# Optimization experiments

Measured on AMD Instinct MI355X. Metric: run time of the kernel, lower is better.

Reference implementation:

```python
import jax, jax.numpy as jnp
import numpy as np

B, S, P = 2, 1024, 1024          # batch, new tokens, cached (past) tokens
H, NQ, NKV, D = 4096, 32, 8, 128  # hidden, q heads, kv heads, head dim
G = NQ // NKV                     # GQA group size
SCALE = 1.0 / np.sqrt(D)


def _make_rope(positions, dim, base=10000.0):
    inv = 1.0 / (base ** (np.arange(0, dim, 2, dtype=np.float32) / dim))
    freqs = positions[:, None].astype(np.float32) * inv[None, :]
    emb = np.concatenate([freqs, freqs], axis=-1)  # [S, D]
    return jnp.asarray(np.cos(emb)), jnp.asarray(np.sin(emb))


def setup_inputs() -> dict:
    key = jax.random.key(0)
    ks = jax.random.split(key, 5)
    hidden_states = jax.random.normal(ks[0], (B, S, H), jnp.float32)
    w_qkv = jax.random.normal(ks[1], (H, (NQ + 2 * NKV) * D), jnp.float32) * 0.02
    w_o = jax.random.normal(ks[2], (NQ * D, H), jnp.float32) * 0.02
    cos, sin = _make_rope(np.arange(P, P + S), D)  # new tokens at positions P..P+S-1
    k_cache = jax.random.normal(ks[3], (B, P, NKV, D), jnp.float32)
    v_cache = jax.random.normal(ks[4], (B, P, NKV, D), jnp.float32)
    return dict(hidden_states=hidden_states, w_qkv=w_qkv, w_o=w_o,
                cos=cos, sin=sin, k_cache=k_cache, v_cache=v_cache)


def _rotate_half(x):
    x1, x2 = jnp.split(x, 2, axis=-1)
    return jnp.concatenate([-x2, x1], axis=-1)


def _apply_rope(x, cos, sin):
    # x: [B,S,N,D]; cos/sin: [S,D]
    return x * cos[None, :, None, :] + _rotate_half(x) * sin[None, :, None, :]


def reference(hidden_states, w_qkv, w_o, cos, sin, k_cache, v_cache):
    # fused QKV projection
    qkv = hidden_states @ w_qkv                       # [B,S,(NQ+2*NKV)*D]
    q, k, v = jnp.split(qkv, [NQ * D, (NQ + NKV) * D], axis=-1)
    q = q.reshape(B, S, NQ, D)
    k = k.reshape(B, S, NKV, D)
    v = v.reshape(B, S, NKV, D)
    # inline RoPE on q and k
    q = _apply_rope(q, cos, sin)
    k = _apply_rope(k, cos, sin)
    # append new k/v to the KV cache (quant_bits=0 path: fp cache)
    k_all = jnp.concatenate([k_cache, k], axis=1)     # [B,T,NKV,D], T = P+S
    v_all = jnp.concatenate([v_cache, v], axis=1)
    # GQA attention: group q heads per kv head
    qg = q.reshape(B, S, NKV, G, D)
    scores = jnp.einsum('bsngd,btnd->bngst', qg, k_all) * SCALE  # [B,NKV,G,S,T]
    # causal mask offset by cache length: new token s sees t <= s + P
    t_idx = jnp.arange(P + S)
    s_idx = jnp.arange(S)
    mask = t_idx[None, :] <= (s_idx[:, None] + P)      # [S,T]
    neg = jnp.asarray(jnp.finfo(scores.dtype).min, scores.dtype)
    scores = jnp.where(mask[None, None, None], scores, neg)
    probs = jax.nn.softmax(scores, axis=-1)
    out = jnp.einsum('bngst,btnd->bsngd', probs, v_all).reshape(B, S, NQ * D)
    return out @ w_o                                   # [B,S,H]
```

## Files before the change

kernel.cpp:

```cpp
#include <hip/hip_runtime.h>
#include <hip/hip_bf16.h>
#include <cstdint>
#include <cstddef>

#define B_    2
#define S_    1024
#define P_    1024
#define T_    2048
#define H_    4096
#define NQ_   32
#define NKV_  8
#define D_    128
#define QKVN_ 6144
#define SCALE_ 0.08838834764831845f

typedef unsigned short u16;
typedef short  bf16x8 __attribute__((ext_vector_type(8)));
typedef float  f32x4  __attribute__((ext_vector_type(4)));

__device__ __forceinline__ float bf2f(u16 u) {
  union { unsigned u; float f; } x; x.u = ((unsigned)u) << 16; return x.f;
}
__device__ __forceinline__ u16 f2bf(float f) {
  union { float f; unsigned u; } x; x.f = f;
  unsigned r = (x.u + 0x7fffu + ((x.u >> 16) & 1u)) >> 16;
  return (u16)r;
}

__device__ __forceinline__ void gload16(const void* g, void* l) {
  __builtin_amdgcn_global_load_lds(
      (const __attribute__((address_space(1))) unsigned int*)g,
      (__attribute__((address_space(3))) unsigned int*)l, 16, 0, 0);
}

__global__ void k_f32_to_bf16(const float* __restrict__ in, u16* __restrict__ out, int n4) {
  int i = blockIdx.x * blockDim.x + threadIdx.x;
  if (i >= n4) return;
  float4 v = ((const float4*)in)[i];
  union { u16 s[4]; uint2 v; } o;
  o.s[0] = f2bf(v.x); o.s[1] = f2bf(v.y); o.s[2] = f2bf(v.z); o.s[3] = f2bf(v.w);
  ((uint2*)out)[i] = o.v;
}

__global__ void k_wtrans(const float* __restrict__ w, u16* __restrict__ wt, int K, int N) {
  __shared__ __align__(16) u16 tile[64][66];
  const int n0 = blockIdx.x * 64;
  const int k0 = blockIdx.y * 64;
  const int tid = threadIdx.x;
  const int c = tid & 63;
  const int r4 = tid >> 6;
#pragma unroll
  for (int i = 0; i < 16; ++i) {
    int rr = r4 * 16 + i;
    tile[rr][c] = f2bf(w[(size_t)(k0 + rr) * N + n0 + c]);
  }
  __syncthreads();
#pragma unroll
  for (int i = 0; i < 16; ++i) {
    int rr = r4 * 16 + i;
    wt[(size_t)(n0 + rr) * K + k0 + c] = tile[c][rr];
  }
}

template<bool BF16OUT>
__global__ __launch_bounds__(256, 2)
void k_gemm(const u16* __restrict__ A, const u16* __restrict__ Bt,
            void* __restrict__ Cv, int M, int N, int K) {
  __shared__ __align__(16) u16 As[128 * 64];
  __shared__ __align__(16) u16 Bs[128 * 64];
  const int tid = threadIdx.x;
  const int lane = tid & 63;
  const int wv = tid >> 6;
  const int wm = wv >> 1, wn = wv & 1;
  const int m0 = blockIdx.y * 128;
  const int n0 = blockIdx.x * 128;
  const int l15 = lane & 15, l4 = lane >> 4;

  f32x4 acc[4][4] = {};
  const int nk = K >> 6;
  int srow[4], scol[4];
#pragma unroll
  for (int i = 0; i < 4; ++i) {
    int chunk = tid + i * 256;
    srow[i] = chunk >> 3;
    scol[i] = (chunk & 7) ^ (srow[i] & 7);
  }
  for (int kt = 0; kt < nk; ++kt) {
    __syncthreads();
#pragma unroll
    for (int i = 0; i < 4; ++i) {
      int chunk = tid + i * 256;
      gload16(A  + (size_t)(m0 + srow[i]) * K + kt * 64 + scol[i] * 8, &As[chunk * 8]);
      gload16(Bt + (size_t)(n0 + srow[i]) * K + kt * 64 + scol[i] * 8, &Bs[chunk * 8]);
    }
    __syncthreads();
    bf16x8 af[4][2], bfr[4][2];
#pragma unroll
    for (int mt = 0; mt < 4; ++mt) {
      int r = wm * 64 + mt * 16 + l15;
#pragma unroll
      for (int ks = 0; ks < 2; ++ks) {
        int cc = (ks * 4 + l4) ^ (r & 7);
        af[mt][ks] = *(const bf16x8*)(&As[r * 64 + cc * 8]);
      }
    }
#pragma unroll
    for (int nt = 0; nt < 4; ++nt) {
      int r = wn * 64 + nt * 16 + l15;
#pragma unroll
      for (int ks = 0; ks < 2; ++ks) {
        int cc = (ks * 4 + l4) ^ (r & 7);
        bfr[nt][ks] = *(const bf16x8*)(&Bs[r * 64 + cc * 8]);
      }
    }
#pragma unroll
    for (int mt = 0; mt < 4; ++mt)
#pragma unroll
      for (int nt = 0; nt < 4; ++nt)
#pragma unroll
        for (int ks = 0; ks < 2; ++ks)
          acc[mt][nt] = __builtin_amdgcn_mfma_f32_16x16x32_bf16(
              af[mt][ks], bfr[nt][ks], acc[mt][nt], 0, 0, 0);
  }
#pragma unroll
  for (int mt = 0; mt < 4; ++mt)
#pragma unroll
    for (int nt = 0; nt < 4; ++nt)
#pragma unroll
      for (int i = 0; i < 4; ++i) {
        int row = m0 + wm * 64 + mt * 16 + l4 * 4 + i;
        int col = n0 + wn * 64 + nt * 16 + l15;
        size_t off = (size_t)row * N + col;
        if (BF16OUT) ((u16*)Cv)[off] = f2bf(acc[mt][nt][i]);
        else         ((float*)Cv)[off] = acc[mt][nt][i];
      }
}

__global__ void k_rope_scatter(const u16* __restrict__ qkv,
                               const float* __restrict__ cosb, const float* __restrict__ sinb,
                               const float* __restrict__ kcache,
                               u16* __restrict__ Q, u16* __restrict__ Kall) {
  const int gsz = gridDim.x * blockDim.x;
  const int i0 = blockIdx.x * blockDim.x + threadIdx.x;
  for (int i = i0; i < B_ * S_ * NQ_ * 64; i += gsz) {
    int d = i & 63, hh = (i >> 6) & 31, s = (i >> 11) & 1023, b = i >> 21;
    const u16* row = qkv + (size_t)(b * S_ + s) * QKVN_ + hh * D_;
    float x1 = bf2f(row[d]), x2 = bf2f(row[d + 64]);
    float c = cosb[s * D_ + d], sn = sinb[s * D_ + d];
    u16* q = Q + (size_t)((b * NQ_ + hh) * S_ + s) * D_;
    q[d]      = f2bf((x1 * c - x2 * sn) * SCALE_);
    q[d + 64] = f2bf((x2 * c + x1 * sn) * SCALE_);
  }
  for (int i = i0; i < B_ * S_ * NKV_ * 64; i += gsz) {
    int d = i & 63, kh = (i >> 6) & 7, s = (i >> 9) & 1023, b = i >> 19;
    const u16* row = qkv + (size_t)(b * S_ + s) * QKVN_ + NQ_ * D_ + kh * D_;
    float x1 = bf2f(row[d]), x2 = bf2f(row[d + 64]);
    float c = cosb[s * D_ + d], sn = sinb[s * D_ + d];
    u16* kd = Kall + (size_t)((b * NKV_ + kh) * T_ + P_ + s) * D_;
    kd[d]      = f2bf(x1 * c - x2 * sn);
    kd[d + 64] = f2bf(x2 * c + x1 * sn);
  }
  for (int i = i0; i < B_ * P_ * NKV_ * D_; i += gsz) {
    int d = i & 127, kh = (i >> 7) & 7, t = (i >> 10) & 1023, b = i >> 20;
    float x = kcache[(size_t)((b * P_ + t) * NKV_ + kh) * D_ + d];
    Kall[(size_t)((b * NKV_ + kh) * T_ + t) * D_ + d] = f2bf(x);
  }
}

__global__ void k_vbuild(const u16* __restrict__ qkv, const float* __restrict__ vcache,
                         u16* __restrict__ Vt) {
  __shared__ __align__(16) u16 tile[64][66];
  const int t0 = blockIdx.x * 64;
  const int d0 = blockIdx.y * 64;
  const int bkh = blockIdx.z;
  const int b = bkh >> 3, kh = bkh & 7;
  const int tid = threadIdx.x;
  const int c = tid & 63, r4 = tid >> 6;
#pragma unroll
  for (int i = 0; i < 16; ++i) {
    int rr = r4 * 16 + i;
    int t = t0 + rr;
    float x;
    if (t < P_) x = vcache[(size_t)((b * P_ + t) * NKV_ + kh) * D_ + d0 + c];
    else        x = bf2f(qkv[(size_t)(b * S_ + (t - P_)) * QKVN_ + (NQ_ + NKV_) * D_ + kh * D_ + d0 + c]);
    tile[rr][c] = f2bf(x);
  }
  __syncthreads();
  u16* out = Vt + ((size_t)(b * NKV_ + kh) * D_ + d0) * T_ + t0;
#pragma unroll
  for (int i = 0; i < 16; ++i) {
    int rr = r4 * 16 + i;
    out[(size_t)rr * T_ + c] = tile[c][rr];
  }
}

__global__ __launch_bounds__(256, 2)
void k_attn(const u16* __restrict__ Q, const u16* __restrict__ Kall,
            const u16* __restrict__ Vt, u16* __restrict__ O) {
  __shared__ __align__(16) u16 Ks[64 * 128];
  __shared__ __align__(16) u16 Vs[128 * 64];
  __shared__ __align__(16) u16 Ps[4][32 * 64];
  const int sb = blockIdx.x;
  const int h  = blockIdx.y;
  const int b  = blockIdx.z;
  const int kh = h >> 2;
  const int tid = threadIdx.x;
  const int lane = tid & 63, wv = tid >> 6;
  const int l15 = lane & 15, l4 = lane >> 4;
  const int s0 = sb * 128;
  const int rowbase = s0 + wv * 32;

  const u16* qbase = Q + (size_t)(b * NQ_ + h) * S_ * D_;
  bf16x8 qf[2][4];
#pragma unroll
  for (int mt = 0; mt < 2; ++mt)
#pragma unroll
    for (int ks = 0; ks < 4; ++ks)
      qf[mt][ks] = *(const bf16x8*)(qbase + (size_t)(rowbase + mt * 16 + l15) * D_ + ks * 32 + l4 * 8);

  f32x4 acco[2][8] = {};
  float mrun[2][4], lrun[2][4];
#pragma unroll
  for (int mt = 0; mt < 2; ++mt)
#pragma unroll
    for (int i = 0; i < 4; ++i) { mrun[mt][i] = -1e30f; lrun[mt][i] = 0.f; }

  const u16* kbase = Kall + (size_t)(b * NKV_ + kh) * T_ * D_;
  const u16* vbase = Vt   + (size_t)(b * NKV_ + kh) * D_ * T_;
  const int ntiles = min(32, 2 * sb + 18);

  for (int tt = 0; tt < ntiles; ++tt) {
    const int t0 = tt * 64;
    __syncthreads();
#pragma unroll
    for (int i = 0; i < 4; ++i) {
      int chunk = tid + i * 256;
      int kr = chunk >> 4, kc = chunk & 15;
      gload16(kbase + (size_t)(t0 + kr) * D_ + (kc ^ (kr & 7)) * 8, &Ks[chunk * 8]);
      int vr = chunk >> 3, vc = chunk & 7;
      gload16(vbase + (size_t)vr * T_ + t0 + (vc ^ (vr & 7)) * 8, &Vs[chunk * 8]);
    }
    __syncthreads();

    f32x4 accs[2][4] = {};
#pragma unroll
    for (int tb = 0; tb < 4; ++tb) {
      int r = tb * 16 + l15;
#pragma unroll
      for (int ks = 0; ks < 4; ++ks) {
        int cc = (ks * 4 + l4) ^ (r & 7);
        bf16x8 kf = *(const bf16x8*)(&Ks[r * 128 + cc * 8]);
#pragma unroll
        for (int mt = 0; mt < 2; ++mt)
          accs[mt][tb] = __builtin_amdgcn_mfma_f32_16x16x32_bf16(qf[mt][ks], kf, accs[mt][tb], 0, 0, 0);
      }
    }
    if (tt >= 2 * sb + 16) {
#pragma unroll
      for (int mt = 0; mt < 2; ++mt)
#pragma unroll
        for (int tb = 0; tb < 4; ++tb)
#pragma unroll
          for (int i = 0; i < 4; ++i) {
            int srow = rowbase + mt * 16 + l4 * 4 + i;
            int tcol = t0 + tb * 16 + l15;
            if (tcol > srow + P_) accs[mt][tb][i] = -1e30f;
          }
    }
#pragma unroll
    for (int mt = 0; mt < 2; ++mt) {
      float al[4];
#pragma unroll
      for (int i = 0; i < 4; ++i) {
        float v = fmaxf(fmaxf(accs[mt][0][i], accs[mt][1][i]),
                        fmaxf(accs[mt][2][i], accs[mt][3][i]));
        v = fmaxf(v, __shfl_xor(v, 1));
        v = fmaxf(v, __shfl_xor(v, 2));
        v = fmaxf(v, __shfl_xor(v, 4));
        v = fmaxf(v, __shfl_xor(v, 8));
        float mn = fmaxf(mrun[mt][i], v);
        al[i] = __expf(mrun[mt][i] - mn);
        mrun[mt][i] = mn;
      }
      float rs[4] = {0.f, 0.f, 0.f, 0.f};
#pragma unroll
      for (int tb = 0; tb < 4; ++tb)
#pragma unroll
        for (int i = 0; i < 4; ++i) {
          float p = __expf(accs[mt][tb][i] - mrun[mt][i]);
          accs[mt][tb][i] = p;
          rs[i] += p;
        }
#pragma unroll
      for (int i = 0; i < 4; ++i) {
        rs[i] += __shfl_xor(rs[i], 1);
        rs[i] += __shfl_xor(rs[i], 2);
        rs[i] += __shfl_xor(rs[i], 4);
        rs[i] += __shfl_xor(rs[i], 8);
        lrun[mt][i] = lrun[mt][i] * al[i] + rs[i];
      }
#pragma unroll
      for (int db = 0; db < 8; ++db)
#pragma unroll
        for (int i = 0; i < 4; ++i)
          acco[mt][db][i] *= al[i];
#pragma unroll
      for (int tb = 0; tb < 4; ++tb)
#pragma unroll
        for (int i = 0; i < 4; ++i) {
          int r = mt * 16 + l4 * 4 + i;
          int col = tb * 16 + l15;
          int cc = (col >> 3) ^ (r & 7);
          Ps[wv][r * 64 + cc * 8 + (col & 7)] = f2bf(accs[mt][tb][i]);
        }
    }
#pragma unroll
    for (int ks = 0; ks < 2; ++ks) {
      bf16x8 pf[2];
#pragma unroll
      for (int mt = 0; mt < 2; ++mt) {
        int r = mt * 16 + l15;
        int cc = (ks * 4 + l4) ^ (r & 7);
        pf[mt] = *(const bf16x8*)(&Ps[wv][r * 64 + cc * 8]);
      }
#pragma unroll
      for (int db = 0; db < 8; ++db) {
        int r = db * 16 + l15;
        int cc = (ks * 4 + l4) ^ (r & 7);
        bf16x8 vf = *(const bf16x8*)(&Vs[r * 64 + cc * 8]);
#pragma unroll
        for (int mt = 0; mt < 2; ++mt)
          acco[mt][db] = __builtin_amdgcn_mfma_f32_16x16x32_bf16(pf[mt], vf, acco[mt][db], 0, 0, 0);
      }
    }
  }
#pragma unroll
  for (int mt = 0; mt < 2; ++mt)
#pragma unroll
    for (int db = 0; db < 8; ++db)
#pragma unroll
      for (int i = 0; i < 4; ++i) {
        int srow = rowbase + mt * 16 + l4 * 4 + i;
        int d = db * 16 + l15;
        float o = acco[mt][db][i] / lrun[mt][i];
        O[(size_t)(b * S_ + srow) * (NQ_ * D_) + h * D_ + d] = f2bf(o);
      }
}

extern "C" void kernel_launch(void* const* d_in, const int* in_sizes, int n_in,
                              void* d_out, int out_size, void* d_ws, size_t ws_size,
                              hipStream_t stream) {
  const float* hidden = (const float*)d_in[0];
  const float* w_qkv  = (const float*)d_in[1];
  const float* w_o    = (const float*)d_in[2];
  const float* cosb   = (const float*)d_in[3];
  const float* sinb   = (const float*)d_in[4];
  const float* kc     = (const float*)d_in[5];
  const float* vc     = (const float*)d_in[6];
  float* out = (float*)d_out;

  char* ws = (char*)d_ws;
  u16* wqkvt = (u16*)(ws + 0);
  u16* hid   = (u16*)(ws + 50331648);
  u16* qkv   = (u16*)(ws + 67108864);
  u16* wot   = (u16*)(ws + 50331648);
  u16* qrope = (u16*)(ws + 92274688);
  u16* kall  = (u16*)(ws + 109051904);
  u16* vallt = (u16*)(ws + 117440512);
  u16* attno = (u16*)(ws + 125829120);

  k_wtrans<<<dim3(QKVN_ / 64, H_ / 64), 256, 0, stream>>>(w_qkv, wqkvt, H_, QKVN_);
  k_f32_to_bf16<<<(B_ * S_ * H_ / 4 + 255) / 256, 256, 0, stream>>>(hidden, hid, B_ * S_ * H_ / 4);
  k_gemm<true><<<dim3(QKVN_ / 128, (B_ * S_) / 128), 256, 0, stream>>>(
      hid, wqkvt, qkv, B_ * S_, QKVN_, H_);
  k_rope_scatter<<<2048, 256, 0, stream>>>(qkv, cosb, sinb, kc, qrope, kall);
  k_vbuild<<<dim3(T_ / 64, D_ / 64, B_ * NKV_), 256, 0, stream>>>(qkv, vc, vallt);
  k_wtrans<<<dim3(H_ / 64, H_ / 64), 256, 0, stream>>>(w_o, wot, H_, H_);
  k_attn<<<dim3(S_ / 128, NQ_, B_), 256, 0, stream>>>(qrope, kall, vallt, attno);
  k_gemm<false><<<dim3(H_ / 128, (B_ * S_) / 128), 256, 0, stream>>>(
      attno, wot, out, B_ * S_, H_, H_);
}
```

Baseline: 579.0 us.

## Double-buffer K/V tiles in attention and skip softmax rescale when max is stable

The attention kernel now double-buffers its K and V shared-memory tiles, prefetching the next tile with async loads and waiting with partial vmcnt so global loads overlap the MFMA work. It adds s_setprio around the MFMA phases and scheduling barriers. Online softmax now skips the running-max update and accumulator rescale when every row's new max is within 8 of the old one, which removes many exps and multiplies. Shared memory doubles for K/V, which may cut occupancy below two blocks per CU, and the lazy rescale lets unnormalized probabilities grow up to e^8 before the bf16 cast.

```diff
diff --git a/kernel.cpp b/kernel.cpp
--- a/kernel.cpp
+++ b/kernel.cpp
@@ -197,8 +197,8 @@
 __global__ __launch_bounds__(256, 2)
 void k_attn(const u16* __restrict__ Q, const u16* __restrict__ Kall,
             const u16* __restrict__ Vt, u16* __restrict__ O) {
-  __shared__ __align__(16) u16 Ks[64 * 128];
-  __shared__ __align__(16) u16 Vs[128 * 64];
+  __shared__ __align__(16) u16 Ks[2][64 * 128];
+  __shared__ __align__(16) u16 Vs[2][128 * 64];
   __shared__ __align__(16) u16 Ps[4][32 * 64];
   const int sb = blockIdx.x;
   const int h  = blockIdx.y;
@@ -210,51 +210,71 @@
   const int s0 = sb * 128;
   const int rowbase = s0 + wv * 32;
 
-  const u16* qbase = Q + (size_t)(b * NQ_ + h) * S_ * D_;
-  bf16x8 qf[2][4];
-#pragma unroll
-  for (int mt = 0; mt < 2; ++mt)
-#pragma unroll
-    for (int ks = 0; ks < 4; ++ks)
-      qf[mt][ks] = *(const bf16x8*)(qbase + (size_t)(rowbase + mt * 16 + l15) * D_ + ks * 32 + l4 * 8);
-
-  f32x4 acco[2][8] = {};
-  float mrun[2][4], lrun[2][4];
-#pragma unroll
-  for (int mt = 0; mt < 2; ++mt)
-#pragma unroll
-    for (int i = 0; i < 4; ++i) { mrun[mt][i] = -1e30f; lrun[mt][i] = 0.f; }
-
   const u16* kbase = Kall + (size_t)(b * NKV_ + kh) * T_ * D_;
   const u16* vbase = Vt   + (size_t)(b * NKV_ + kh) * D_ * T_;
   const int ntiles = min(32, 2 * sb + 18);
 
-  for (int tt = 0; tt < ntiles; ++tt) {
-    const int t0 = tt * 64;
-    __syncthreads();
+  int kr[4], kc[4], vr[4], vc[4];
+#pragma unroll
+  for (int i = 0; i < 4; ++i) {
+    int chunk = tid + i * 256;
+    kr[i] = chunk >> 4; kc[i] = (chunk & 15) ^ (kr[i] & 7);
+    vr[i] = chunk >> 3; vc[i] = (chunk & 7)  ^ (vr[i] & 7);
+  }
+  auto stage = [&](int buf, int t0) {
 #pragma unroll
     for (int i = 0; i < 4; ++i) {
       int chunk = tid + i * 256;
-      int kr = chunk >> 4, kc = chunk & 15;
-      gload16(kbase + (size_t)(t0 + kr) * D_ + (kc ^ (kr & 7)) * 8, &Ks[chunk * 8]);
-      int vr = chunk >> 3, vc = chunk & 7;
-      gload16(vbase + (size_t)vr * T_ + t0 + (vc ^ (vr & 7)) * 8, &Vs[chunk * 8]);
-    }
-    __syncthreads();
+      gload16(kbase + (size_t)(t0 + kr[i]) * D_ + kc[i] * 8, &Ks[buf][chunk * 8]);
+      gload16(vbase + (size_t)vr[i] * T_ + t0 + vc[i] * 8,  &Vs[buf][chunk * 8]);
+    }
+  };
+
+  const u16* qbase = Q + (size_t)(b * NQ_ + h) * S_ * D_;
+  bf16x8 qf[2][4];
+#pragma unroll
+  for (int mt = 0; mt < 2; ++mt)
+#pragma unroll
+    for (int ks = 0; ks < 4; ++ks)
+      qf[mt][ks] = *(const bf16x8*)(qbase + (size_t)(rowbase + mt * 16 + l15) * D_ + ks * 32 + l4 * 8);
+
+  f32x4 acco[2][8] = {};
+  float mrun[2][4], lrun[2][4];
+#pragma unroll
+  for (int mt = 0; mt < 2; ++mt)
+#pragma unroll
+    for (int i = 0; i < 4; ++i) { mrun[mt][i] = -1e30f; lrun[mt][i] = 0.f; }
+
+  stage(0, 0);
+
+  for (int tt = 0; tt < ntiles; ++tt) {
+    const int cur = tt & 1;
+    const int t0 = tt * 64;
+    if (tt + 1 < ntiles) {
+      stage(cur ^ 1, (tt + 1) * 64);
+      asm volatile("s_waitcnt vmcnt(8)" ::: "memory");
+    } else {
+      asm volatile("s_waitcnt vmcnt(0)" ::: "memory");
+    }
+    __builtin_amdgcn_sched_barrier(0);
+    __builtin_amdgcn_s_barrier();
+    __builtin_amdgcn_sched_barrier(0);
 
     f32x4 accs[2][4] = {};
+    __builtin_amdgcn_s_setprio(1);
 #pragma unroll
     for (int tb = 0; tb < 4; ++tb) {
       int r = tb * 16 + l15;
 #pragma unroll
       for (int ks = 0; ks < 4; ++ks) {
         int cc = (ks * 4 + l4) ^ (r & 7);
-        bf16x8 kf = *(const bf16x8*)(&Ks[r * 128 + cc * 8]);
+        bf16x8 kf = *(const bf16x8*)(&Ks[cur][r * 128 + cc * 8]);
 #pragma unroll
         for (int mt = 0; mt < 2; ++mt)
           accs[mt][tb] = __builtin_amdgcn_mfma_f32_16x16x32_bf16(qf[mt][ks], kf, accs[mt][tb], 0, 0, 0);
       }
     }
+    __builtin_amdgcn_s_setprio(0);
     if (tt >= 2 * sb + 16) {
 #pragma unroll
       for (int mt = 0; mt < 2; ++mt)
@@ -269,7 +289,7 @@
     }
 #pragma unroll
     for (int mt = 0; mt < 2; ++mt) {
-      float al[4];
+      float vmax[4];
 #pragma unroll
       for (int i = 0; i < 4; ++i) {
         float v = fmaxf(fmaxf(accs[mt][0][i], accs[mt][1][i]),
@@ -278,9 +298,22 @@
         v = fmaxf(v, __shfl_xor(v, 2));
         v = fmaxf(v, __shfl_xor(v, 4));
         v = fmaxf(v, __shfl_xor(v, 8));
-        float mn = fmaxf(mrun[mt][i], v);
-        al[i] = __expf(mrun[mt][i] - mn);
-        mrun[mt][i] = mn;
+        vmax[i] = v;
+      }
+      bool ok = true;
+#pragma unroll
+      for (int i = 0; i < 4; ++i) ok = ok && (vmax[i] <= mrun[mt][i] + 8.f);
+      if (!__all(ok)) {
+#pragma unroll
+        for (int i = 0; i < 4; ++i) {
+          float mn = fmaxf(mrun[mt][i], vmax[i]);
+          float al = __expf(mrun[mt][i] - mn);
+          mrun[mt][i] = mn;
+          lrun[mt][i] *= al;
+#pragma unroll
+          for (int db = 0; db < 8; ++db)
+            acco[mt][db][i] *= al;
+        }
       }
       float rs[4] = {0.f, 0.f, 0.f, 0.f};
 #pragma unroll
@@ -297,13 +330,8 @@
         rs[i] += __shfl_xor(rs[i], 2);
         rs[i] += __shfl_xor(rs[i], 4);
         rs[i] += __shfl_xor(rs[i], 8);
-        lrun[mt][i] = lrun[mt][i] * al[i] + rs[i];
-      }
-#pragma unroll
-      for (int db = 0; db < 8; ++db)
-#pragma unroll
-        for (int i = 0; i < 4; ++i)
-          acco[mt][db][i] *= al[i];
+        lrun[mt][i] += rs[i];
+      }
 #pragma unroll
       for (int tb = 0; tb < 4; ++tb)
 #pragma unroll
@@ -314,6 +342,7 @@
           Ps[wv][r * 64 + cc * 8 + (col & 7)] = f2bf(accs[mt][tb][i]);
         }
     }
+    __builtin_amdgcn_s_setprio(1);
 #pragma unroll
     for (int ks = 0; ks < 2; ++ks) {
       bf16x8 pf[2];
@@ -327,12 +356,16 @@
       for (int db = 0; db < 8; ++db) {
         int r = db * 16 + l15;
         int cc = (ks * 4 + l4) ^ (r & 7);
-        bf16x8 vf = *(const bf16x8*)(&Vs[r * 64 + cc * 8]);
+        bf16x8 vf = *(const bf16x8*)(&Vs[cur][r * 64 + cc * 8]);
 #pragma unroll
         for (int mt = 0; mt < 2; ++mt)
           acco[mt][db] = __builtin_amdgcn_mfma_f32_16x16x32_bf16(pf[mt], vf, acco[mt][db], 0, 0, 0);
       }
     }
+    __builtin_amdgcn_s_setprio(0);
+    __builtin_amdgcn_sched_barrier(0);
+    __builtin_amdgcn_s_barrier();
+    __builtin_amdgcn_sched_barrier(0);
   }
 #pragma unroll
   for (int mt = 0; mt < 2; ++mt)
```

Result: faster. 555.3 us (-4.1%).
